# Optimization experiments

Measured on AMD Instinct MI355X. Metric: run time of the kernel, lower is better.

## Reference

```python
import jax, jax.numpy as jnp
import numpy as np

N = 100000
E = 3_200_000
H = 64
R = 2
NEG = 0.01   # leaky_relu default slope
EPS = 1e-5   # BatchNorm eps


def leaky(x):
    return jnp.where(x > 0, x, NEG * x)


def bn(x, g, b, m, v):
    # BatchNorm1d in eval mode (running statistics)
    return (x - m) * jax.lax.rsqrt(v + EPS) * g + b


def setup_inputs() -> dict:
    key = jax.random.key(0)
    ks = jax.random.split(key, 16)
    d = {}
    d["des"] = jax.random.normal(ks[0], (N, 768), jnp.float32)
    d["num"] = jax.random.normal(ks[1], (N, 5), jnp.float32)
    d["cat"] = jax.random.normal(ks[2], (N, 6), jnp.float32)
    d["edge_index"] = jax.random.randint(ks[3], (2, E), 0, N)
    d["edge_type"] = jax.random.randint(ks[4], (E,), 0, R)

    def lin(k, o, i):
        return (jax.random.normal(k, (o, i), jnp.float32) / np.float32(np.sqrt(i)))

    # projection heads: Linear + BatchNorm1d params
    d["des_W"] = lin(ks[5], H, 768); d["des_b"] = jnp.zeros((H,), jnp.float32)
    d["num_W"] = lin(ks[6], H, 5);   d["num_b"] = jnp.zeros((H,), jnp.float32)
    d["cat_W"] = lin(ks[7], H, 6);   d["cat_b"] = jnp.zeros((H,), jnp.float32)
    for name, kk in (("des", ks[8]), ("num", ks[9]), ("cat", ks[10])):
        d[name + "_g"] = jnp.ones((H,), jnp.float32)
        d[name + "_beta"] = jnp.zeros((H,), jnp.float32)
        d[name + "_m"] = 0.1 * jax.random.normal(kk, (H,), jnp.float32)
        d[name + "_v"] = jnp.ones((H,), jnp.float32)
    # RGCN relation weights [R, in, out] (used as F.linear(x, W[r]) -> x @ W[r].T)
    d["rgcn_W"] = jax.random.normal(ks[11], (R, H, H), jnp.float32) / np.float32(np.sqrt(H))
    # classifier
    d["cls_W1"] = lin(ks[12], H // 2, H); d["cls_b1"] = jnp.zeros((H // 2,), jnp.float32)
    d["cls_W2"] = lin(ks[13], 2, H // 2); d["cls_b2"] = jnp.zeros((2,), jnp.float32)
    return d


def reference(des, num, cat, edge_index, edge_type,
              des_W, des_b, des_g, des_beta, des_m, des_v,
              num_W, num_b, num_g, num_beta, num_m, num_v,
              cat_W, cat_b, cat_g, cat_beta, cat_m, cat_v,
              rgcn_W, cls_W1, cls_b1, cls_W2, cls_b2):
    # feature fusion: three Linear+BN+LeakyReLU branches summed
    x = leaky(bn(des @ des_W.T + des_b, des_g, des_beta, des_m, des_v))
    x = x + leaky(bn(num @ num_W.T + num_b, num_g, num_beta, num_m, num_v))
    x = x + leaky(bn(cat @ cat_W.T + cat_b, cat_g, cat_beta, cat_m, cat_v))

    # SimpleRGCNConv: per-relation linear transform + masked scatter-mean over edges
    src, dst = edge_index[0], edge_index[1]  # PyG: row=source, col=target
    n = x.shape[0]
    acc = jnp.zeros((n, H), x.dtype)
    for r in range(R):
        x_r = x @ rgcn_W[r].T                       # F.linear(x, weight[r])
        mask = (edge_type == r).astype(x.dtype)     # [E]
        msg = x_r[src] * mask[:, None]              # gather + mask
        s = jax.ops.segment_sum(msg, dst, num_segments=n)
        cnt = jax.ops.segment_sum(mask, dst, num_segments=n)
        acc = acc + s / jnp.maximum(cnt, 1.0)[:, None]  # mean; 0 for isolated nodes
    x = leaky(acc / R)  # mean over relations

    # dropout in eval mode is identity; classifier
    h = leaky(x @ cls_W1.T + cls_b1)
    return h @ cls_W2.T + cls_b2
```

## Files before the change

### kernel.cpp

```cpp
#include <hip/hip_runtime.h>

typedef unsigned int u32;
typedef unsigned short u16;

#define NEG 0.01f
#define BN_EPS 1e-5f

typedef __attribute__((ext_vector_type(8))) short bf16x8;
typedef __attribute__((ext_vector_type(4))) float f32x4;

__device__ __forceinline__ float bl(u32 u){ union { u32 i; float f; } c; c.i = u << 16; return c.f; }
__device__ __forceinline__ float bh(u32 u){ union { u32 i; float f; } c; c.i = u & 0xFFFF0000u; return c.f; }
__device__ __forceinline__ u16 f2b(float f){
  union { float f; u32 i; } c; c.f = f;
  u32 t = c.i + 0x7FFFu + ((c.i >> 16) & 1u);
  return (u16)(t >> 16);
}
__device__ __forceinline__ float leaky(float v){ return v > 0.f ? v : NEG * v; }

__global__ __launch_bounds__(256) void k_hist_prep(
    const int* __restrict__ ei, const int* __restrict__ et, int E, int HB,
    int* __restrict__ deg2,
    const float* __restrict__ desWf, const float* __restrict__ rgcnW,
    const float* __restrict__ W1, u16* __restrict__ tab)
{
  int bid = blockIdx.x;
  if (bid < HB) {
    int e = bid * 256 + threadIdx.x;
    if (e < E) atomicAdd(&deg2[ei[E + e] * 2 + et[e]], 1);
  } else {
    int i = (bid - HB) * 256 + threadIdx.x;
    if (i < 49152) {
      tab[i] = f2b(desWf[i]);
    } else if (i < 57344) {
      int j = i - 49152;
      int h = j >> 7, k = j & 127;
      tab[i] = f2b(rgcnW[(k >= 64 ? 4096 : 0) + h * 64 + (k & 63)]);
    } else if (i < 59392) {
      tab[i] = f2b(W1[i - 57344]);
    }
  }
}

__global__ __launch_bounds__(256) void k_fuse_scan(
    const float* __restrict__ des, const float* __restrict__ nump, const float* __restrict__ catp,
    const u16* __restrict__ desW16, const float* __restrict__ desB,
    const float* __restrict__ numW, const float* __restrict__ numB,
    const float* __restrict__ catW, const float* __restrict__ catB,
    const float* __restrict__ dg, const float* __restrict__ dbe, const float* __restrict__ dm, const float* __restrict__ dv,
    const float* __restrict__ ng, const float* __restrict__ nbe, const float* __restrict__ nm, const float* __restrict__ nv,
    const float* __restrict__ cg, const float* __restrict__ cbe, const float* __restrict__ cm, const float* __restrict__ cv,
    u16* __restrict__ x16, int n,
    const int* __restrict__ deg2, int* __restrict__ offs2, int M)
{
  const int tid  = threadIdx.x;
  const int lane = tid & 63;
  const int w    = tid >> 6;

  if (blockIdx.x == 0) {
    __shared__ int wsum[4];
    __shared__ int carry;
    if (tid == 0) carry = 0;
    __syncthreads();
    for (int base = 0; base < M; base += 1024) {
      int idx = base + tid * 4;
      int4 v = {0, 0, 0, 0};
      if (idx < M) v = *(const int4*)(deg2 + idx);
      int s4 = v.x + v.y + v.z + v.w;
      int s = s4;
      #pragma unroll
      for (int o = 1; o < 64; o <<= 1) { int t = __shfl_up(s, o); if (lane >= o) s += t; }
      if (lane == 63) wsum[w] = s;
      __syncthreads();
      if (tid == 0) {
        int a = wsum[0];
        a += wsum[1]; wsum[1] = a;
        a += wsum[2]; wsum[2] = a;
        a += wsum[3]; wsum[3] = a;
      }
      __syncthreads();
      int wbase = (w == 0) ? 0 : wsum[w - 1];
      int ebase = carry + wbase + (s - s4);
      if (idx < M) {
        int4 o4;
        o4.x = ebase;
        o4.y = ebase + v.x;
        o4.z = ebase + v.x + v.y;
        o4.w = ebase + v.x + v.y + v.z;
        *(int4*)(offs2 + idx) = o4;
      }
      __syncthreads();
      if (tid == 0) carry += wsum[3];
      __syncthreads();
    }
    if (tid == 0) offs2[M] = carry;
    return;
  }

  __shared__ float ync[64][66];

  const int quad = lane >> 4;
  const int l15  = lane & 15;
  const int rowbase = (blockIdx.x - 1) * 64 + 16 * w;

  {
    float nw[5], cw[6];
    #pragma unroll
    for (int j = 0; j < 5; ++j) nw[j] = numW[lane * 5 + j];
    #pragma unroll
    for (int j = 0; j < 6; ++j) cw[j] = catW[lane * 6 + j];
    float An = ng[lane] * rsqrtf(nv[lane] + BN_EPS);
    float Bn = (numB[lane] - nm[lane]) * An + nbe[lane];
    float Ac = cg[lane] * rsqrtf(cv[lane] + BN_EPS);
    float Bc = (catB[lane] - cm[lane]) * Ac + cbe[lane];
    for (int m = 0; m < 16; ++m) {
      int node = rowbase + m; if (node > n - 1) node = n - 1;
      float yn = 0.f, yc = 0.f;
      #pragma unroll
      for (int j = 0; j < 5; ++j) yn = fmaf(nump[node * 5 + j], nw[j], yn);
      #pragma unroll
      for (int j = 0; j < 6; ++j) yc = fmaf(catp[node * 6 + j], cw[j], yc);
      ync[16 * w + m][lane] = leaky(yn * An + Bn) + leaky(yc * Ac + Bc);
    }
  }

  float Ad4[4], Bd4[4];
  #pragma unroll
  for (int t = 0; t < 4; ++t) {
    int nn = 16 * t + l15;
    float A = dg[nn] * rsqrtf(dv[nn] + BN_EPS);
    Ad4[t] = A;
    Bd4[t] = (desB[nn] - dm[nn]) * A + dbe[nn];
  }
  __syncthreads();

  int rowA = rowbase + l15; if (rowA > n - 1) rowA = n - 1;
  const float* aP  = des + (size_t)rowA * 768 + quad * 8;
  const u16* b0P = desW16 + (size_t)(l15)      * 768 + quad * 8;
  const u16* b1P = desW16 + (size_t)(16 + l15) * 768 + quad * 8;
  const u16* b2P = desW16 + (size_t)(32 + l15) * 768 + quad * 8;
  const u16* b3P = desW16 + (size_t)(48 + l15) * 768 + quad * 8;

  f32x4 acc[4];
  #pragma unroll
  for (int t = 0; t < 4; ++t) acc[t] = (f32x4){0.f, 0.f, 0.f, 0.f};

  #pragma unroll 2
  for (int k = 0; k < 768; k += 32) {
    float4 x0 = *(const float4*)(aP + k);
    float4 x1 = *(const float4*)(aP + k + 4);
    bf16x8 a;
    a[0] = (short)f2b(x0.x); a[1] = (short)f2b(x0.y);
    a[2] = (short)f2b(x0.z); a[3] = (short)f2b(x0.w);
    a[4] = (short)f2b(x1.x); a[5] = (short)f2b(x1.y);
    a[6] = (short)f2b(x1.z); a[7] = (short)f2b(x1.w);
    acc[0] = __builtin_amdgcn_mfma_f32_16x16x32_bf16(a, *(const bf16x8*)(b0P + k), acc[0], 0, 0, 0);
    acc[1] = __builtin_amdgcn_mfma_f32_16x16x32_bf16(a, *(const bf16x8*)(b1P + k), acc[1], 0, 0, 0);
    acc[2] = __builtin_amdgcn_mfma_f32_16x16x32_bf16(a, *(const bf16x8*)(b2P + k), acc[2], 0, 0, 0);
    acc[3] = __builtin_amdgcn_mfma_f32_16x16x32_bf16(a, *(const bf16x8*)(b3P + k), acc[3], 0, 0, 0);
  }

  #pragma unroll
  for (int t = 0; t < 4; ++t) {
    #pragma unroll
    for (int r = 0; r < 4; ++r) {
      int m = quad * 4 + r;
      int node = rowbase + m;
      if (node < n) {
        int nn = 16 * t + l15;
        float v = leaky(acc[t][r] * Ad4[t] + Bd4[t]) + ync[16 * w + m][nn];
        x16[(size_t)node * 64 + nn] = f2b(v);
      }
    }
  }
}

__global__ void k_place(const int* __restrict__ ei, const int* __restrict__ et, int E,
                        const int* __restrict__ offs2, int* __restrict__ cur2, int* __restrict__ packed)
{
  int e = blockIdx.x * 256 + threadIdx.x;
  if (e < E) {
    int bin = ei[E + e] * 2 + et[e];
    int pos = offs2[bin] + atomicAdd(&cur2[bin], 1);
    packed[pos] = ei[e];
  }
}

__global__ __launch_bounds__(256) void k_agg(
    const u16* __restrict__ x16, const int* __restrict__ offs2, const int* __restrict__ packed,
    u32* __restrict__ agg, int n)
{
  const int tid = threadIdx.x, lane = tid & 63, w = tid >> 6;
  const int c = lane & 31, half = lane >> 5;

  for (int nd = blockIdx.x * 4 + w; nd < n; nd += gridDim.x * 4) {
    int o0 = offs2[nd * 2], o1 = offs2[nd * 2 + 1], o2 = offs2[nd * 2 + 2];
    float aE[2], aO[2];

    #pragma unroll
    for (int rel = 0; rel < 2; ++rel) {
      int beg = rel ? o1 : o0;
      int end = rel ? o2 : o1;
      float accE = 0.f, accO = 0.f;
      for (int j0 = beg; j0 < end; j0 += 64) {
        int idx = j0 + lane;
        int p = (idx < end) ? packed[idx] : 0;
        p = (p < 0) ? 0 : ((p > n - 1) ? (n - 1) : p);
        int cn = end - j0; if (cn > 64) cn = 64;
        int t = 0;
        for (; t + 16 <= cn; t += 16) {
          int s0 = __shfl(p, t      + half);
          int s1 = __shfl(p, t + 2  + half);
          int s2 = __shfl(p, t + 4  + half);
          int s3 = __shfl(p, t + 6  + half);
          int s4 = __shfl(p, t + 8  + half);
          int s5 = __shfl(p, t + 10 + half);
          int s6 = __shfl(p, t + 12 + half);
          int s7 = __shfl(p, t + 14 + half);
          u32 v0 = *(const u32*)(x16 + (size_t)s0 * 64 + 2 * c);
          u32 v1 = *(const u32*)(x16 + (size_t)s1 * 64 + 2 * c);
          u32 v2 = *(const u32*)(x16 + (size_t)s2 * 64 + 2 * c);
          u32 v3 = *(const u32*)(x16 + (size_t)s3 * 64 + 2 * c);
          u32 v4 = *(const u32*)(x16 + (size_t)s4 * 64 + 2 * c);
          u32 v5 = *(const u32*)(x16 + (size_t)s5 * 64 + 2 * c);
          u32 v6 = *(const u32*)(x16 + (size_t)s6 * 64 + 2 * c);
          u32 v7 = *(const u32*)(x16 + (size_t)s7 * 64 + 2 * c);
          accE += ((bl(v0) + bl(v1)) + (bl(v2) + bl(v3))) + ((bl(v4) + bl(v5)) + (bl(v6) + bl(v7)));
          accO += ((bh(v0) + bh(v1)) + (bh(v2) + bh(v3))) + ((bh(v4) + bh(v5)) + (bh(v6) + bh(v7)));
        }
        for (; t + 8 <= cn; t += 8) {
          int s0 = __shfl(p, t     + half);
          int s1 = __shfl(p, t + 2 + half);
          int s2 = __shfl(p, t + 4 + half);
          int s3 = __shfl(p, t + 6 + half);
          u32 v0 = *(const u32*)(x16 + (size_t)s0 * 64 + 2 * c);
          u32 v1 = *(const u32*)(x16 + (size_t)s1 * 64 + 2 * c);
          u32 v2 = *(const u32*)(x16 + (size_t)s2 * 64 + 2 * c);
          u32 v3 = *(const u32*)(x16 + (size_t)s3 * 64 + 2 * c);
          accE += (bl(v0) + bl(v1)) + (bl(v2) + bl(v3));
          accO += (bh(v0) + bh(v1)) + (bh(v2) + bh(v3));
        }
        for (; t + 2 <= cn; t += 2) {
          int s0 = __shfl(p, t + half);
          u32 v0 = *(const u32*)(x16 + (size_t)s0 * 64 + 2 * c);
          accE += bl(v0); accO += bh(v0);
        }
        if (t < cn) {
          int s0 = __shfl(p, t);
          if (half == 0) {
            u32 v0 = *(const u32*)(x16 + (size_t)s0 * 64 + 2 * c);
            accE += bl(v0); accO += bh(v0);
          }
        }
      }
      accE += __shfl_xor(accE, 32);
      accO += __shfl_xor(accO, 32);
      int cnt = end - beg;
      float sc = 1.f / (float)(cnt > 1 ? cnt : 1);
      aE[rel] = accE * sc;
      aO[rel] = accO * sc;
    }

    float sE = half ? aE[1] : aE[0];
    float sO = half ? aO[1] : aO[0];
    agg[(size_t)nd * 64 + lane] = (u32)f2b(sE) | ((u32)f2b(sO) << 16);
  }
}

__global__ __launch_bounds__(256) void k_mlp(
    const u32* __restrict__ agg, const u16* __restrict__ Wmlp, const u16* __restrict__ W1p,
    const float* __restrict__ b1, const float* __restrict__ W2, const float* __restrict__ b2,
    float2* __restrict__ out, int n)
{
  __shared__ __align__(16) u16 h1[4][16][72];
  __shared__ float h2[4][16][34];

  const int tid = threadIdx.x, lane = tid & 63, w = tid >> 6;
  const int quad = lane >> 4, l15 = lane & 15;
  const int rowbase = blockIdx.x * 64 + 16 * w;

  int rowA = rowbase + l15; if (rowA > n - 1) rowA = n - 1;
  const u16* aRow = (const u16*)(agg + (size_t)rowA * 64);

  f32x4 acc[4];
  #pragma unroll
  for (int t = 0; t < 4; ++t) acc[t] = (f32x4){0.f, 0.f, 0.f, 0.f};
  #pragma unroll
  for (int ks = 0; ks < 4; ++ks) {
    bf16x8 a = *(const bf16x8*)(aRow + ks * 32 + quad * 8);
    #pragma unroll
    for (int t = 0; t < 4; ++t) {
      bf16x8 b = *(const bf16x8*)(Wmlp + (size_t)(16 * t + l15) * 128 + ks * 32 + quad * 8);
      acc[t] = __builtin_amdgcn_mfma_f32_16x16x32_bf16(a, b, acc[t], 0, 0, 0);
    }
  }
  #pragma unroll
  for (int t = 0; t < 4; ++t)
    #pragma unroll
    for (int r = 0; r < 4; ++r) {
      int m = quad * 4 + r;
      h1[w][m][16 * t + l15] = f2b(leaky(0.5f * acc[t][r]));
    }
  __syncthreads();

  f32x4 acc2[2];
  acc2[0] = (f32x4){0.f, 0.f, 0.f, 0.f};
  acc2[1] = (f32x4){0.f, 0.f, 0.f, 0.f};
  #pragma unroll
  for (int ks = 0; ks < 2; ++ks) {
    bf16x8 a = *(const bf16x8*)(&h1[w][l15][ks * 32 + quad * 8]);
    #pragma unroll
    for (int t = 0; t < 2; ++t) {
      bf16x8 b = *(const bf16x8*)(W1p + (size_t)(16 * t + l15) * 64 + ks * 32 + quad * 8);
      acc2[t] = __builtin_amdgcn_mfma_f32_16x16x32_bf16(a, b, acc2[t], 0, 0, 0);
    }
  }
  #pragma unroll
  for (int t = 0; t < 2; ++t)
    #pragma unroll
    for (int r = 0; r < 4; ++r) {
      int m = quad * 4 + r;
      int j = 16 * t + l15;
      h2[w][m][j] = leaky(acc2[t][r] + b1[j]);
    }
  __syncthreads();

  float t0 = 0.f, t1 = 0.f;
  #pragma unroll
  for (int jj = 0; jj < 8; ++jj) {
    int j = quad * 8 + jj;
    float hv = h2[w][l15][j];
    t0 = fmaf(hv, W2[j], t0);
    t1 = fmaf(hv, W2[32 + j], t1);
  }
  t0 += __shfl_xor(t0, 16); t0 += __shfl_xor(t0, 32);
  t1 += __shfl_xor(t1, 16); t1 += __shfl_xor(t1, 32);
  int node = rowbase + l15;
  if (quad == 0 && node < n) {
    float2 q; q.x = t0 + b2[0]; q.y = t1 + b2[1];
    out[node] = q;
  }
}

extern "C" void kernel_launch(void* const* d_in, const int* in_sizes, int n_in,
                              void* d_out, int out_size, void* d_ws, size_t ws_size,
                              hipStream_t stream)
{
  const float* des  = (const float*)d_in[0];
  const float* nump = (const float*)d_in[1];
  const float* catp = (const float*)d_in[2];
  const int* ei   = (const int*)d_in[3];
  const int* et   = (const int*)d_in[4];
  const float* desW = (const float*)d_in[5];
  const float* desB = (const float*)d_in[6];
  const float* numW = (const float*)d_in[7];
  const float* numB = (const float*)d_in[8];
  const float* catW = (const float*)d_in[9];
  const float* catB = (const float*)d_in[10];
  const float* dg  = (const float*)d_in[11];
  const float* dbe = (const float*)d_in[12];
  const float* dm  = (const float*)d_in[13];
  const float* dv  = (const float*)d_in[14];
  const float* ng  = (const float*)d_in[15];
  const float* nbe = (const float*)d_in[16];
  const float* nm  = (const float*)d_in[17];
  const float* nv  = (const float*)d_in[18];
  const float* cg  = (const float*)d_in[19];
  const float* cbe = (const float*)d_in[20];
  const float* cm  = (const float*)d_in[21];
  const float* cv  = (const float*)d_in[22];
  const float* rgcnW = (const float*)d_in[23];
  const float* W1 = (const float*)d_in[24];
  const float* b1 = (const float*)d_in[25];
  const float* W2 = (const float*)d_in[26];
  const float* b2 = (const float*)d_in[27];

  const int N = in_sizes[1] / 5;
  const int E = in_sizes[4];
  const int M = 2 * N;

  char* ws = (char*)d_ws;
  u16* tab    = (u16*)ws;                  size_t off = (size_t)59392 * 2;
  off = (off + 255) & ~(size_t)255;
  u16* x16    = (u16*)(ws + off);          off += (size_t)N * 64 * 2;
  u32* agg    = (u32*)(ws + off);          off += (size_t)N * 64 * 4;
  int* deg2   = (int*)(ws + off);          off += (size_t)M * 4;
  int* cur2   = (int*)(ws + off);          off += (size_t)M * 4;
  int* offs2  = (int*)(ws + off);          off += (size_t)(M + 1) * 4;
  off = (off + 255) & ~(size_t)255;
  int* packed = (int*)(ws + off);

  u16* desW16 = tab;
  u16* Wmlp   = tab + 49152;
  u16* W1p    = tab + 57344;

  hipMemsetAsync(deg2, 0, (size_t)M * 8, stream);

  const int HB = (E + 255) / 256;
  const int PB = (59392 + 255) / 256;
  k_hist_prep<<<HB + PB, 256, 0, stream>>>(ei, et, E, HB, deg2, desW, rgcnW, W1, tab);

  const int FB = (N + 63) / 64;
  k_fuse_scan<<<FB + 1, 256, 0, stream>>>(des, nump, catp, desW16, desB, numW, numB, catW, catB,
                                          dg, dbe, dm, dv, ng, nbe, nm, nv, cg, cbe, cm, cv,
                                          x16, N, deg2, offs2, M);

  k_place<<<(E + 255) / 256, 256, 0, stream>>>(ei, et, E, offs2, cur2, packed);
  k_agg<<<2048, 256, 0, stream>>>(x16, offs2, packed, agg, N);
  k_mlp<<<(N + 63) / 64, 256, 0, stream>>>(agg, Wmlp, W1p, b1, W2, b2, (float2*)d_out, N);
}
```

Before: 951.4 us.

## Pre-convert des to bf16 in MFMA fragment layout and repack desW

Adds blocks to the histogram/prep kernel that convert the 100000x768 fp32 des matrix to bf16 and store it tiled in the exact MFMA A-fragment order. The des weight matrix is repacked the same way, so the fused GEMM kernel does one contiguous 16-byte load per fragment with no conversion. This moves the fp32 to bf16 conversion out of the GEMM loop, but adds a full extra pass: des is read once as fp32 and written as bf16, then read again by the GEMM.

```diff
diff --git a/kernel.cpp b/kernel.cpp
--- a/kernel.cpp
+++ b/kernel.cpp
@@ -19,19 +19,23 @@
 __device__ __forceinline__ float leaky(float v){ return v > 0.f ? v : NEG * v; }
 
 __global__ __launch_bounds__(256) void k_hist_prep(
-    const int* __restrict__ ei, const int* __restrict__ et, int E, int HB,
+    const int* __restrict__ ei, const int* __restrict__ et, int E, int HB, int PB,
     int* __restrict__ deg2,
     const float* __restrict__ desWf, const float* __restrict__ rgcnW,
-    const float* __restrict__ W1, u16* __restrict__ tab)
+    const float* __restrict__ W1, u16* __restrict__ tab,
+    const float* __restrict__ des, u16* __restrict__ des16, int n)
 {
   int bid = blockIdx.x;
   if (bid < HB) {
     int e = bid * 256 + threadIdx.x;
     if (e < E) atomicAdd(&deg2[ei[E + e] * 2 + et[e]], 1);
-  } else {
+  } else if (bid < HB + PB) {
     int i = (bid - HB) * 256 + threadIdx.x;
     if (i < 49152) {
-      tab[i] = f2b(desWf[i]);
+      int j = i & 7, lane = (i >> 3) & 63, t = (i >> 9) & 3, k = i >> 11;
+      int row = 16 * t + (lane & 15);
+      int col = 32 * k + 8 * (lane >> 4) + j;
+      tab[i] = f2b(desWf[row * 768 + col]);
     } else if (i < 57344) {
       int j = i - 49152;
       int h = j >> 7, k = j & 127;
@@ -39,12 +43,35 @@
     } else if (i < 59392) {
       tab[i] = f2b(W1[i - 57344]);
     }
+  } else {
+    int fb = bid - HB - PB;
+    const int tid = threadIdx.x;
+    u16* outb = des16 + (size_t)fb * 49152;
+    #pragma unroll 4
+    for (int it = 0; it < 24; ++it) {
+      int s = it * 256 + tid;
+      int lane = s & 63;
+      int k = (s >> 6) % 24;
+      int w = s / 1536;
+      int row = fb * 64 + 16 * w + (lane & 15);
+      if (row > n - 1) row = n - 1;
+      int col = 32 * k + 8 * (lane >> 4);
+      const float* p = des + (size_t)row * 768 + col;
+      float4 u = *(const float4*)p;
+      float4 v = *(const float4*)(p + 4);
+      int4 o4;
+      o4.x = (int)((u32)f2b(u.x) | ((u32)f2b(u.y) << 16));
+      o4.y = (int)((u32)f2b(u.z) | ((u32)f2b(u.w) << 16));
+      o4.z = (int)((u32)f2b(v.x) | ((u32)f2b(v.y) << 16));
+      o4.w = (int)((u32)f2b(v.z) | ((u32)f2b(v.w) << 16));
+      *(int4*)(outb + (size_t)s * 8) = o4;
+    }
   }
 }
 
 __global__ __launch_bounds__(256) void k_fuse_scan(
-    const float* __restrict__ des, const float* __restrict__ nump, const float* __restrict__ catp,
-    const u16* __restrict__ desW16, const float* __restrict__ desB,
+    const u16* __restrict__ des16, const float* __restrict__ nump, const float* __restrict__ catp,
+    const u16* __restrict__ Wpk, const float* __restrict__ desB,
     const float* __restrict__ numW, const float* __restrict__ numB,
     const float* __restrict__ catW, const float* __restrict__ catB,
     const float* __restrict__ dg, const float* __restrict__ dbe, const float* __restrict__ dm, const float* __restrict__ dv,
@@ -101,7 +128,8 @@
 
   const int quad = lane >> 4;
   const int l15  = lane & 15;
-  const int rowbase = (blockIdx.x - 1) * 64 + 16 * w;
+  const int fb   = blockIdx.x - 1;
+  const int rowbase = fb * 64 + 16 * w;
 
   {
     float nw[5], cw[6];
@@ -134,30 +162,20 @@
   }
   __syncthreads();
 
-  int rowA = rowbase + l15; if (rowA > n - 1) rowA = n - 1;
-  const float* aP  = des + (size_t)rowA * 768 + quad * 8;
-  const u16* b0P = desW16 + (size_t)(l15)      * 768 + quad * 8;
-  const u16* b1P = desW16 + (size_t)(16 + l15) * 768 + quad * 8;
-  const u16* b2P = desW16 + (size_t)(32 + l15) * 768 + quad * 8;
-  const u16* b3P = desW16 + (size_t)(48 + l15) * 768 + quad * 8;
+  const u16* aP = des16 + (size_t)(fb * 4 + w) * 12288 + lane * 8;
+  const u16* bP = Wpk + lane * 8;
 
   f32x4 acc[4];
   #pragma unroll
   for (int t = 0; t < 4; ++t) acc[t] = (f32x4){0.f, 0.f, 0.f, 0.f};
 
-  #pragma unroll 2
-  for (int k = 0; k < 768; k += 32) {
-    float4 x0 = *(const float4*)(aP + k);
-    float4 x1 = *(const float4*)(aP + k + 4);
-    bf16x8 a;
-    a[0] = (short)f2b(x0.x); a[1] = (short)f2b(x0.y);
-    a[2] = (short)f2b(x0.z); a[3] = (short)f2b(x0.w);
-    a[4] = (short)f2b(x1.x); a[5] = (short)f2b(x1.y);
-    a[6] = (short)f2b(x1.z); a[7] = (short)f2b(x1.w);
-    acc[0] = __builtin_amdgcn_mfma_f32_16x16x32_bf16(a, *(const bf16x8*)(b0P + k), acc[0], 0, 0, 0);
-    acc[1] = __builtin_amdgcn_mfma_f32_16x16x32_bf16(a, *(const bf16x8*)(b1P + k), acc[1], 0, 0, 0);
-    acc[2] = __builtin_amdgcn_mfma_f32_16x16x32_bf16(a, *(const bf16x8*)(b2P + k), acc[2], 0, 0, 0);
-    acc[3] = __builtin_amdgcn_mfma_f32_16x16x32_bf16(a, *(const bf16x8*)(b3P + k), acc[3], 0, 0, 0);
+  #pragma unroll 4
+  for (int k = 0; k < 24; ++k) {
+    bf16x8 a = *(const bf16x8*)(aP + k * 512);
+    acc[0] = __builtin_amdgcn_mfma_f32_16x16x32_bf16(a, *(const bf16x8*)(bP + k * 2048       ), acc[0], 0, 0, 0);
+    acc[1] = __builtin_amdgcn_mfma_f32_16x16x32_bf16(a, *(const bf16x8*)(bP + k * 2048 +  512), acc[1], 0, 0, 0);
+    acc[2] = __builtin_amdgcn_mfma_f32_16x16x32_bf16(a, *(const bf16x8*)(bP + k * 2048 + 1024), acc[2], 0, 0, 0);
+    acc[3] = __builtin_amdgcn_mfma_f32_16x16x32_bf16(a, *(const bf16x8*)(bP + k * 2048 + 1536), acc[3], 0, 0, 0);
   }
 
   #pragma unroll
@@ -378,6 +396,7 @@
   const int N = in_sizes[1] / 5;
   const int E = in_sizes[4];
   const int M = 2 * N;
+  const int NB = (N + 63) / 64;
 
   char* ws = (char*)d_ws;
   u16* tab    = (u16*)ws;                  size_t off = (size_t)59392 * 2;
@@ -388,9 +407,11 @@
   int* cur2   = (int*)(ws + off);          off += (size_t)M * 4;
   int* offs2  = (int*)(ws + off);          off += (size_t)(M + 1) * 4;
   off = (off + 255) & ~(size_t)255;
-  int* packed = (int*)(ws + off);
-
-  u16* desW16 = tab;
+  int* packed = (int*)(ws + off);          off += (size_t)E * 4;
+  off = (off + 255) & ~(size_t)255;
+  u16* des16  = (u16*)(ws + off);
+
+  u16* Wpk    = tab;
   u16* Wmlp   = tab + 49152;
   u16* W1p    = tab + 57344;
 
@@ -398,10 +419,11 @@
 
   const int HB = (E + 255) / 256;
   const int PB = (59392 + 255) / 256;
-  k_hist_prep<<<HB + PB, 256, 0, stream>>>(ei, et, E, HB, deg2, desW, rgcnW, W1, tab);
-
-  const int FB = (N + 63) / 64;
-  k_fuse_scan<<<FB + 1, 256, 0, stream>>>(des, nump, catp, desW16, desB, numW, numB, catW, catB,
+  k_hist_prep<<<HB + PB + NB, 256, 0, stream>>>(ei, et, E, HB, PB, deg2,
+                                                desW, rgcnW, W1, tab,
+                                                des, des16, N);
+
+  k_fuse_scan<<<NB + 1, 256, 0, stream>>>(des16, nump, catp, Wpk, desB, numW, numB, catW, catB,
                                           dg, dbe, dm, dv, ng, nbe, nm, nv, cg, cbe, cm, cv,
                                           x16, N, deg2, offs2, M);
 
```

Measured after the change: 1.063 ms. 11.7% more time.

## Stage des tiles in LDS with coalesced loads and pre-pack desW in MFMA fragment order

Applied to the files above, without the earlier changes.

The des GEMM previously had each lane read its own row's 8-float slice straight from global memory, and read B fragments from strided row-major bf16 weights. Now the block loads 64x128 tiles of des with coalesced float4 loads, converts them to bf16 into a padded LDS tile, and feeds the MFMAs from LDS. The prep kernel also stores desW in per-lane fragment order so each B load is one contiguous 16-byte read. The cost is extra __syncthreads per tile and added LDS use, which may lower occupancy.

```diff
diff --git a/kernel.cpp b/kernel.cpp
--- a/kernel.cpp
+++ b/kernel.cpp
@@ -31,7 +31,10 @@
   } else {
     int i = (bid - HB) * 256 + threadIdx.x;
     if (i < 49152) {
-      tab[i] = f2b(desWf[i]);
+      int j = i & 7, lane = (i >> 3) & 63, t = (i >> 9) & 3, k = i >> 11;
+      int row = 16 * t + (lane & 15);
+      int col = 32 * k + 8 * (lane >> 4) + j;
+      tab[i] = f2b(desWf[row * 768 + col]);
     } else if (i < 57344) {
       int j = i - 49152;
       int h = j >> 7, k = j & 127;
@@ -44,7 +47,7 @@
 
 __global__ __launch_bounds__(256) void k_fuse_scan(
     const float* __restrict__ des, const float* __restrict__ nump, const float* __restrict__ catp,
-    const u16* __restrict__ desW16, const float* __restrict__ desB,
+    const u16* __restrict__ Wpk, const float* __restrict__ desB,
     const float* __restrict__ numW, const float* __restrict__ numB,
     const float* __restrict__ catW, const float* __restrict__ catB,
     const float* __restrict__ dg, const float* __restrict__ dbe, const float* __restrict__ dm, const float* __restrict__ dv,
@@ -98,10 +101,12 @@
   }
 
   __shared__ float ync[64][66];
+  __shared__ __align__(16) u16 atile[64 * 136];
 
   const int quad = lane >> 4;
   const int l15  = lane & 15;
-  const int rowbase = (blockIdx.x - 1) * 64 + 16 * w;
+  const int fb   = blockIdx.x - 1;
+  const int rowbase = fb * 64 + 16 * w;
 
   {
     float nw[5], cw[6];
@@ -134,30 +139,40 @@
   }
   __syncthreads();
 
-  int rowA = rowbase + l15; if (rowA > n - 1) rowA = n - 1;
-  const float* aP  = des + (size_t)rowA * 768 + quad * 8;
-  const u16* b0P = desW16 + (size_t)(l15)      * 768 + quad * 8;
-  const u16* b1P = desW16 + (size_t)(16 + l15) * 768 + quad * 8;
-  const u16* b2P = desW16 + (size_t)(32 + l15) * 768 + quad * 8;
-  const u16* b3P = desW16 + (size_t)(48 + l15) * 768 + quad * 8;
+  const u16* bP = Wpk + lane * 8;
 
   f32x4 acc[4];
   #pragma unroll
   for (int t = 0; t < 4; ++t) acc[t] = (f32x4){0.f, 0.f, 0.f, 0.f};
 
-  #pragma unroll 2
-  for (int k = 0; k < 768; k += 32) {
-    float4 x0 = *(const float4*)(aP + k);
-    float4 x1 = *(const float4*)(aP + k + 4);
-    bf16x8 a;
-    a[0] = (short)f2b(x0.x); a[1] = (short)f2b(x0.y);
-    a[2] = (short)f2b(x0.z); a[3] = (short)f2b(x0.w);
-    a[4] = (short)f2b(x1.x); a[5] = (short)f2b(x1.y);
-    a[6] = (short)f2b(x1.z); a[7] = (short)f2b(x1.w);
-    acc[0] = __builtin_amdgcn_mfma_f32_16x16x32_bf16(a, *(const bf16x8*)(b0P + k), acc[0], 0, 0, 0);
-    acc[1] = __builtin_amdgcn_mfma_f32_16x16x32_bf16(a, *(const bf16x8*)(b1P + k), acc[1], 0, 0, 0);
-    acc[2] = __builtin_amdgcn_mfma_f32_16x16x32_bf16(a, *(const bf16x8*)(b2P + k), acc[2], 0, 0, 0);
-    acc[3] = __builtin_amdgcn_mfma_f32_16x16x32_bf16(a, *(const bf16x8*)(b3P + k), acc[3], 0, 0, 0);
+  const int blk64 = fb * 64;
+  for (int tile = 0; tile < 6; ++tile) {
+    if (tile > 0) __syncthreads();
+    #pragma unroll
+    for (int it = 0; it < 4; ++it) {
+      int j  = it * 256 + tid;
+      int r  = j >> 4;
+      int sg = j & 15;
+      int row = blk64 + r; if (row > n - 1) row = n - 1;
+      const float* p = des + (size_t)row * 768 + tile * 128 + sg * 8;
+      float4 u = *(const float4*)p;
+      float4 v = *(const float4*)(p + 4);
+      u32* d = (u32*)(atile + r * 136 + sg * 8);
+      d[0] = (u32)f2b(u.x) | ((u32)f2b(u.y) << 16);
+      d[1] = (u32)f2b(u.z) | ((u32)f2b(u.w) << 16);
+      d[2] = (u32)f2b(v.x) | ((u32)f2b(v.y) << 16);
+      d[3] = (u32)f2b(v.z) | ((u32)f2b(v.w) << 16);
+    }
+    __syncthreads();
+    #pragma unroll
+    for (int kk = 0; kk < 4; ++kk) {
+      bf16x8 a = *(const bf16x8*)(atile + (16 * w + l15) * 136 + kk * 32 + quad * 8);
+      int kg = tile * 4 + kk;
+      acc[0] = __builtin_amdgcn_mfma_f32_16x16x32_bf16(a, *(const bf16x8*)(bP + kg * 2048       ), acc[0], 0, 0, 0);
+      acc[1] = __builtin_amdgcn_mfma_f32_16x16x32_bf16(a, *(const bf16x8*)(bP + kg * 2048 +  512), acc[1], 0, 0, 0);
+      acc[2] = __builtin_amdgcn_mfma_f32_16x16x32_bf16(a, *(const bf16x8*)(bP + kg * 2048 + 1024), acc[2], 0, 0, 0);
+      acc[3] = __builtin_amdgcn_mfma_f32_16x16x32_bf16(a, *(const bf16x8*)(bP + kg * 2048 + 1536), acc[3], 0, 0, 0);
+    }
   }
 
   #pragma unroll
@@ -378,6 +393,7 @@
   const int N = in_sizes[1] / 5;
   const int E = in_sizes[4];
   const int M = 2 * N;
+  const int NB = (N + 63) / 64;
 
   char* ws = (char*)d_ws;
   u16* tab    = (u16*)ws;                  size_t off = (size_t)59392 * 2;
@@ -390,7 +406,7 @@
   off = (off + 255) & ~(size_t)255;
   int* packed = (int*)(ws + off);
 
-  u16* desW16 = tab;
+  u16* Wpk    = tab;
   u16* Wmlp   = tab + 49152;
   u16* W1p    = tab + 57344;
 
@@ -400,8 +416,7 @@
   const int PB = (59392 + 255) / 256;
   k_hist_prep<<<HB + PB, 256, 0, stream>>>(ei, et, E, HB, deg2, desW, rgcnW, W1, tab);
 
-  const int FB = (N + 63) / 64;
-  k_fuse_scan<<<FB + 1, 256, 0, stream>>>(des, nump, catp, desW16, desB, numW, numB, catW, catB,
+  k_fuse_scan<<<NB + 1, 256, 0, stream>>>(des, nump, catp, Wpk, desB, numW, numB, catW, catB,
                                           dg, dbe, dm, dv, ng, nbe, nm, nv, cg, cbe, cm, cv,
                                           x16, N, deg2, offs2, M);
 
```

Result: no change. 942.0 us (-1.0%).
